# Kernel optimization log

Hardware: AMD Instinct MI355X
Metric: run time of the kernel (lower is better)

## Reference

```python
import jax, jax.numpy as jnp
import numpy as np

N_ENT = 50000
N_REL = 200
DIM = 128
N_BASES = 4
NUM_RELATIONS = 2 * N_REL  # RGCNConv num_relations
E = 200000
S = 20000


def rgcn_conv(x, edge_index, edge_type, edge_norm, basis, att, root, bias, n_nodes):
    """RGCNConv with basis decomposition, aggr='mean'.
    x: [N, Din]; basis: [B, Din, Dout]; att: [R, B]; root: [Din, Dout]; bias: [Dout].
    """
    src, dst = edge_index[0], edge_index[1]
    x_j = x[src]                      # [E, Din] gather
    att_e = att[edge_type]            # [E, B]
    # message: x_j @ (att_e @ basis) without materializing per-edge [Din,Dout] weights
    msg = jnp.einsum('ei,bio,eb->eo', x_j, basis, att_e)  # [E, Dout]
    msg = msg * edge_norm[:, None]
    agg = jax.ops.segment_sum(msg, dst, num_segments=n_nodes)            # [N, Dout]
    cnt = jax.ops.segment_sum(jnp.ones_like(edge_norm), dst, num_segments=n_nodes)
    agg = agg / jnp.maximum(cnt, 1.0)[:, None]            # mean aggregation
    return agg + x @ root + bias


def setup_inputs() -> dict:
    key = jax.random.key(0)
    ks = jax.random.split(key, 20)
    d = {}
    d['entity'] = jnp.arange(N_ENT, dtype=jnp.int64) if jax.config.read('jax_enable_x64') else jnp.arange(N_ENT, dtype=jnp.int32)
    d['edge_index'] = jax.random.randint(ks[0], (2, E), 0, N_ENT)
    d['edge_type'] = jax.random.randint(ks[1], (E,), 0, NUM_RELATIONS)
    d['edge_norm'] = jax.random.uniform(ks[2], (E,), dtype=jnp.float32)
    d['samples'] = jax.random.randint(ks[3], (S, 3), 0, N_REL)
    d['DAD_rel'] = jax.random.normal(ks[4], (N_REL, N_REL), dtype=jnp.float32) * 0.05
    # learned parameters
    d['entity_emb'] = jax.random.normal(ks[5], (N_ENT, DIM), dtype=jnp.float32) * 0.02
    d['relation_emb'] = jax.random.normal(ks[6], (N_REL, DIM), dtype=jnp.float32) * 0.02
    d['entity_context_tab'] = jax.random.normal(ks[7], (N_ENT, DIM), dtype=jnp.float32) * 0.02
    d['relation_context_tab'] = jax.random.normal(ks[8], (N_REL, DIM), dtype=jnp.float32) * 0.02
    d['relation_gcn_weight'] = jax.random.normal(ks[9], (DIM, DIM), dtype=jnp.float32) * 0.02
    d['gate_entity'] = jax.random.uniform(ks[10], (DIM,), dtype=jnp.float32)
    d['gate_relation'] = jax.random.uniform(ks[11], (DIM,), dtype=jnp.float32)
    d['basis1'] = jax.random.normal(ks[12], (N_BASES, DIM, DIM), dtype=jnp.float32) * 0.02
    d['att1'] = jax.random.normal(ks[13], (NUM_RELATIONS, N_BASES), dtype=jnp.float32) * 0.1
    d['root1'] = jax.random.normal(ks[14], (DIM, DIM), dtype=jnp.float32) * 0.02
    d['bias1'] = jnp.zeros((DIM,), dtype=jnp.float32)
    d['basis2'] = jax.random.normal(ks[15], (N_BASES, DIM, DIM), dtype=jnp.float32) * 0.02
    d['att2'] = jax.random.normal(ks[16], (NUM_RELATIONS, N_BASES), dtype=jnp.float32) * 0.1
    d['root2'] = jax.random.normal(ks[17], (DIM, DIM), dtype=jnp.float32) * 0.02
    d['bias2'] = jnp.zeros((DIM,), dtype=jnp.float32)
    return d


def reference(entity, edge_index, edge_type, edge_norm, samples, DAD_rel,
              entity_emb, relation_emb, entity_context_tab, relation_context_tab,
              relation_gcn_weight, gate_entity, gate_relation,
              basis1, att1, root1, bias1, basis2, att2, root2, bias2):
    n_nodes = entity.shape[0]
    ent_ctx = entity_context_tab[entity]                  # [N, D]
    rel_ctx = relation_context_tab                        # arange over all relations -> full table
    ent_ctx = jax.nn.relu(rgcn_conv(ent_ctx, edge_index, edge_type, edge_norm,
                                    basis1, att1, root1, bias1, n_nodes))
    ent_ctx = jax.nn.relu(rgcn_conv(ent_ctx, edge_index, edge_type, edge_norm,
                                    basis2, att2, root2, bias2, n_nodes))
    rel_ctx = jax.nn.relu((DAD_rel @ rel_ctx) @ relation_gcn_weight)
    ge = jax.nn.sigmoid(gate_entity)
    gr = jax.nn.sigmoid(gate_relation)
    h, r, t = samples[:, 0], samples[:, 1], samples[:, 2]
    head_o = ge * entity_emb[h] + (1.0 - ge) * ent_ctx[h]
    rel_o = gr * relation_emb[r] + (1.0 - gr) * rel_ctx[r]
    tail_o = ge * entity_emb[t] + (1.0 - ge) * ent_ctx[t]
    return jnp.stack([head_o, rel_o, tail_o])             # [3, S, D]
```

## Files before the change

### kernel.cpp

```cpp
#include <hip/hip_runtime.h>
#include <hip/hip_bf16.h>

typedef short s8v  __attribute__((ext_vector_type(8)));
typedef float f16v __attribute__((ext_vector_type(16)));

__device__ __forceinline__ unsigned short f2bf(float x) {
    unsigned u = __float_as_uint(x);
    unsigned r = ((u >> 16) & 1u) + 0x7FFFu;
    return (unsigned short)((u + r) >> 16);
}
__device__ __forceinline__ float bf2f(unsigned short h) {
    return __uint_as_float(((unsigned)h) << 16);
}

__global__ __launch_bounds__(256) void prep_kernel(
    const float* __restrict__ basis1, const float* __restrict__ root1,
    const float* __restrict__ basis2, const float* __restrict__ root2,
    unsigned short* __restrict__ Bp1h, unsigned short* __restrict__ Bp2h,
    const int* __restrict__ edge_index, int* __restrict__ deg, int E,
    const float* __restrict__ tab, const int* __restrict__ entity,
    unsigned short* __restrict__ X0h, unsigned short* __restrict__ X0l, int N,
    const float* __restrict__ DAD, const float* __restrict__ rtab,
    const float* __restrict__ Wrel, float* __restrict__ Rc, int NR,
    int b1, int b2, int b3)
{
    __shared__ float smem[384];
    const int b = blockIdx.x, tid = threadIdx.x;

    if (b < b1) {
        float* part = smem;
        float* r1s  = smem + 256;
        int r = b;
        int o = tid & 127, q = tid >> 7;
        float s = 0.f;
        for (int j = q; j < NR; j += 2)
            s = fmaf(DAD[r * NR + j], rtab[j * 128 + o], s);
        part[q * 128 + o] = s;
        __syncthreads();
        if (tid < 128) r1s[tid] = part[tid] + part[128 + tid];
        __syncthreads();
        float s2 = 0.f;
        #pragma unroll 8
        for (int k = q * 64; k < q * 64 + 64; ++k)
            s2 = fmaf(r1s[k], Wrel[k * 128 + o], s2);
        part[q * 128 + o] = s2;
        __syncthreads();
        if (tid < 128)
            Rc[r * 128 + tid] = fmaxf(part[tid] + part[128 + tid], 0.f);
    } else if (b < b2) {
        int bb = b - b1;
        int layer = bb >= 320;
        int idx = (layer ? bb - 320 : bb) * 256 + tid;
        int n = idx & 127, k = idx >> 7;
        const float* basis = layer ? basis2 : basis1;
        const float* root  = layer ? root2  : root1;
        float v = (k < 512) ? basis[((k & 3) << 14) + ((k >> 2) << 7) + n]
                            : root[((k - 512) << 7) + n];
        size_t pos = (((size_t)(k >> 3) * 128) + n) * 8 + (k & 7);
        (layer ? Bp2h : Bp1h)[pos] = f2bf(v);
    } else if (b < b3) {
        int e = (b - b2) * 256 + tid;
        if (e < E) atomicAdd(&deg[edge_index[E + e]], 1);
    } else {
        int idx = (b - b3) * 256 + tid;
        int n = idx >> 5, l = idx & 31;
        if (n < N) {
            int src = entity[n];
            float4 v = *(const float4*)&tab[(size_t)src * 128 + l * 4];
            ushort4 h, lo;
            h.x = f2bf(v.x); lo.x = f2bf(v.x - bf2f(h.x));
            h.y = f2bf(v.y); lo.y = f2bf(v.y - bf2f(h.y));
            h.z = f2bf(v.z); lo.z = f2bf(v.z - bf2f(h.z));
            h.w = f2bf(v.w); lo.w = f2bf(v.w - bf2f(h.w));
            *(ushort4*)&X0h[(size_t)n * 128 + l * 4] = h;
            *(ushort4*)&X0l[(size_t)n * 128 + l * 4] = lo;
        }
    }
}

__global__ __launch_bounds__(1024) void scanA_kernel(
    const int* __restrict__ deg, int* __restrict__ row_start,
    int* __restrict__ btot, int N)
{
    __shared__ int wtot[16];
    __shared__ int woff[16];
    const int tid = threadIdx.x, lane = tid & 63, wid = tid >> 6;
    int i = blockIdx.x * 1024 + tid;
    int v = (i < N) ? deg[i] : 0;
    int x = v;
    #pragma unroll
    for (int d = 1; d < 64; d <<= 1) {
        int t = __shfl_up(x, d, 64);
        if (lane >= d) x += t;
    }
    if (lane == 63) wtot[wid] = x;
    __syncthreads();
    if (wid == 0 && lane < 16) {
        int s = wtot[lane];
        int y = s;
        #pragma unroll
        for (int d = 1; d < 16; d <<= 1) {
            int t = __shfl_up(y, d, 16);
            if (lane >= d) y += t;
        }
        woff[lane] = y - s;
        if (lane == 15) btot[blockIdx.x] = y;
    }
    __syncthreads();
    if (i < N) row_start[i] = woff[wid] + (x - v);
}

__global__ __launch_bounds__(64) void scanB_kernel(
    const int* __restrict__ btot, int* __restrict__ boff,
    int* __restrict__ row_start, int nB, int N)
{
    int t = threadIdx.x;
    int v = (t < nB) ? btot[t] : 0;
    int x = v;
    #pragma unroll
    for (int d = 1; d < 64; d <<= 1) {
        int u = __shfl_up(x, d, 64);
        if (t >= d) x += u;
    }
    if (t < nB) boff[t] = x - v;
    if (t == nB - 1) row_start[N] = x;
}

__global__ __launch_bounds__(1024) void scanC_kernel(
    int* __restrict__ row_start, int* __restrict__ cursor,
    const int* __restrict__ boff, int N)
{
    int i = blockIdx.x * 1024 + threadIdx.x;
    if (i < N) {
        int r = row_start[i] + boff[blockIdx.x];
        row_start[i] = r;
        cursor[i]    = r;
    }
}

__global__ __launch_bounds__(256) void fill_kernel(
    const int* __restrict__ edge_index, const int* __restrict__ edge_type,
    const float* __restrict__ edge_norm, int* __restrict__ cursor,
    const float* __restrict__ att1, const float* __restrict__ att2,
    int* __restrict__ src_s, float4* __restrict__ an1, float4* __restrict__ an2, int E)
{
    int e = blockIdx.x * 256 + threadIdx.x;
    if (e >= E) return;
    int dst = edge_index[E + e];
    int et  = edge_type[e];
    float n = edge_norm[e];
    int pos = atomicAdd(&cursor[dst], 1);
    src_s[pos] = edge_index[e];
    float4 a1 = *(const float4*)&att1[(size_t)et * 4];
    float4 a2 = *(const float4*)&att2[(size_t)et * 4];
    an1[pos] = make_float4(n * a1.x, n * a1.y, n * a1.z, n * a1.w);
    an2[pos] = make_float4(n * a2.x, n * a2.y, n * a2.z, n * a2.w);
}

__global__ __launch_bounds__(256) void layer_kernel(
    const unsigned short* __restrict__ Xh,
    const unsigned short* __restrict__ Xl,
    const int* __restrict__ row_start,
    const int* __restrict__ src_s,
    const float4* __restrict__ an,
    const unsigned short* __restrict__ Bph,
    const float* __restrict__ bias,
    unsigned short* __restrict__ Xoh,
    unsigned short* __restrict__ Xol,
    int N)
{
    __shared__ unsigned short Whi[80 * 32 * 8];
    __shared__ unsigned short Wlo[16 * 32 * 8];

    const int tid   = threadIdx.x;
    const int node0 = blockIdx.x * 32;

    {
        int g = tid >> 5, l = tid & 31;
        int nb = node0 + g * 4;
        int s0a[4], s1a[4];
        #pragma unroll
        for (int i = 0; i < 4; ++i) {
            int gn = nb + i;
            bool ok = gn < N;
            s0a[i] = ok ? row_start[gn] : 0;
            s1a[i] = ok ? row_start[gn + 1] : 0;
        }
        float acc[4][4][4];
        #pragma unroll
        for (int i = 0; i < 4; ++i)
            #pragma unroll
            for (int d = 0; d < 4; ++d)
                #pragma unroll
                for (int c = 0; c < 4; ++c) acc[i][d][c] = 0.f;

        int need = 0;
        #pragma unroll
        for (int i = 0; i < 4; ++i) need = max(need, s1a[i] - s0a[i]);

        for (int p = 0; p < need; p += 4) {
            #pragma unroll
            for (int i = 0; i < 4; ++i) {
                int q0 = s0a[i] + p;
                if (q0 < s1a[i]) {
                    int se = s1a[i] - 1;
                    int q1 = min(q0 + 1, se);
                    int q2 = min(q0 + 2, se);
                    int q3 = min(q0 + 3, se);
                    int sA = src_s[q0], sB = src_s[q1];
                    int sC = src_s[q2], sD = src_s[q3];
                    float4 aA = an[q0], aB = an[q1];
                    float4 aC = an[q2], aD = an[q3];
                    if (q0 + 1 > se) aB = make_float4(0.f, 0.f, 0.f, 0.f);
                    if (q0 + 2 > se) aC = make_float4(0.f, 0.f, 0.f, 0.f);
                    if (q0 + 3 > se) aD = make_float4(0.f, 0.f, 0.f, 0.f);
                    ushort4 hA = *(const ushort4*)&Xh[(size_t)sA * 128 + (l << 2)];
                    ushort4 hB = *(const ushort4*)&Xh[(size_t)sB * 128 + (l << 2)];
                    ushort4 hC = *(const ushort4*)&Xh[(size_t)sC * 128 + (l << 2)];
                    ushort4 hD = *(const ushort4*)&Xh[(size_t)sD * 128 + (l << 2)];
                    float xsA[4] = {bf2f(hA.x), bf2f(hA.y), bf2f(hA.z), bf2f(hA.w)};
                    float xsB[4] = {bf2f(hB.x), bf2f(hB.y), bf2f(hB.z), bf2f(hB.w)};
                    float xsC[4] = {bf2f(hC.x), bf2f(hC.y), bf2f(hC.z), bf2f(hC.w)};
                    float xsD[4] = {bf2f(hD.x), bf2f(hD.y), bf2f(hD.z), bf2f(hD.w)};
                    #pragma unroll
                    for (int d = 0; d < 4; ++d) {
                        acc[i][d][0] = fmaf(aA.x, xsA[d], fmaf(aB.x, xsB[d], fmaf(aC.x, xsC[d], fmaf(aD.x, xsD[d], acc[i][d][0]))));
                        acc[i][d][1] = fmaf(aA.y, xsA[d], fmaf(aB.y, xsB[d], fmaf(aC.y, xsC[d], fmaf(aD.y, xsD[d], acc[i][d][1]))));
                        acc[i][d][2] = fmaf(aA.z, xsA[d], fmaf(aB.z, xsB[d], fmaf(aC.z, xsC[d], fmaf(aD.z, xsD[d], acc[i][d][2]))));
                        acc[i][d][3] = fmaf(aA.w, xsA[d], fmaf(aB.w, xsB[d], fmaf(aC.w, xsC[d], fmaf(aD.w, xsD[d], acc[i][d][3]))));
                    }
                }
            }
        }
        #pragma unroll
        for (int i = 0; i < 4; ++i) {
            int n = g * 4 + i;
            float inv = 1.0f / fmaxf((float)(s1a[i] - s0a[i]), 1.0f);
            #pragma unroll
            for (int d = 0; d < 4; ++d) {
                int kh   = 2 * l + (d >> 1);
                int slot = n ^ (kh & 31);
                ushort4 h;
                h.x = f2bf(acc[i][d][0] * inv);
                h.y = f2bf(acc[i][d][1] * inv);
                h.z = f2bf(acc[i][d][2] * inv);
                h.w = f2bf(acc[i][d][3] * inv);
                *(ushort4*)&Whi[(kh * 32 + slot) * 8 + (d & 1) * 4] = h;
            }
        }
    }

    {
        int r  = tid >> 3;
        int kq = (tid & 7) * 16;
        int gn = node0 + r;
        #pragma unroll
        for (int i = 0; i < 2; ++i) {
            int kh   = 64 + (tid & 7) * 2 + i;
            int slot = r ^ (kh & 31);
            s8v h8 = {0,0,0,0,0,0,0,0}, l8 = {0,0,0,0,0,0,0,0};
            if (gn < N) {
                h8 = *(const s8v*)&Xh[(size_t)gn * 128 + kq + i * 8];
                l8 = *(const s8v*)&Xl[(size_t)gn * 128 + kq + i * 8];
            }
            *(s8v*)&Whi[(kh * 32 + slot) * 8] = h8;
            *(s8v*)&Wlo[((kh - 64) * 32 + slot) * 8] = l8;
        }
    }
    __syncthreads();

    const int lane = tid & 63, wv = tid >> 6;
    const int m    = lane & 31;
    const int kh8  = lane >> 5;
    const int c0   = wv << 5;

    f16v acc;
    #pragma unroll
    for (int i = 0; i < 16; ++i) acc[i] = 0.f;

    s8v Bb[2][4];
    auto loadB4 = [&](int g, int buf) {
        #pragma unroll
        for (int q = 0; q < 4; ++q) {
            int khg = (g * 4 + q) * 2 + kh8;
            size_t off = ((size_t)khg * 128 + c0 + m) * 8;
            Bb[buf][q] = *(const s8v*)&Bph[off];
        }
    };
    loadB4(0, 0);

    #pragma unroll
    for (int g = 0; g < 10; ++g) {
        int buf = g & 1;
        if (g < 9) loadB4(g + 1, buf ^ 1);
        #pragma unroll
        for (int q = 0; q < 4; ++q) {
            int s    = g * 4 + q;
            int khg  = s * 2 + kh8;
            int slot = m ^ (khg & 31);
            s8v aH = *(const s8v*)&Whi[(khg * 32 + slot) * 8];
            if (s >= 32) {
                s8v aL = *(const s8v*)&Wlo[((khg - 64) * 32 + slot) * 8];
                acc = __builtin_amdgcn_mfma_f32_32x32x16_bf16(aL, Bb[buf][q], acc, 0, 0, 0);
            }
            acc = __builtin_amdgcn_mfma_f32_32x32x16_bf16(aH, Bb[buf][q], acc, 0, 0, 0);
        }
    }

    int gc = c0 + m;
    float bv = bias[gc];
    const int rbase = kh8 << 2;
    #pragma unroll
    for (int reg = 0; reg < 16; ++reg) {
        int gr = node0 + rbase + (reg & 3) + ((reg >> 2) << 3);
        if (gr < N) {
            float v = fmaxf(acc[reg] + bv, 0.f);
            unsigned short h = f2bf(v);
            Xoh[(size_t)gr * 128 + gc] = h;
            Xol[(size_t)gr * 128 + gc] = f2bf(v - bf2f(h));
        }
    }
}

__global__ __launch_bounds__(256) void output_kernel(
    const int* __restrict__ samples,
    const float* __restrict__ gate_e,
    const float* __restrict__ gate_r,
    const float* __restrict__ ent_emb,
    const float* __restrict__ rel_emb,
    const unsigned short* __restrict__ ctx2h,
    const unsigned short* __restrict__ ctx2l,
    const float* __restrict__ relctx,
    float* __restrict__ out, int S)
{
    int s = blockIdx.x * 2 + (threadIdx.x >> 7);
    if (s >= S) return;
    int p = blockIdx.y;
    int o = threadIdx.x & 127;
    float v;
    if (p == 1) {
        int idx = samples[s * 3 + 1];
        float g = 1.0f / (1.0f + __expf(-gate_r[o]));
        v = g * rel_emb[idx * 128 + o] + (1.0f - g) * relctx[idx * 128 + o];
    } else {
        int idx = samples[s * 3 + (p == 0 ? 0 : 2)];
        float g = 1.0f / (1.0f + __expf(-gate_e[o]));
        float c = bf2f(ctx2h[(size_t)idx * 128 + o]) + bf2f(ctx2l[(size_t)idx * 128 + o]);
        v = g * ent_emb[(size_t)idx * 128 + o] + (1.0f - g) * c;
    }
    out[(size_t)p * S * 128 + (size_t)s * 128 + o] = v;
}

extern "C" void kernel_launch(void* const* d_in, const int* in_sizes, int n_in,
                              void* d_out, int out_size, void* d_ws, size_t ws_size,
                              hipStream_t stream)
{
    const int*   entity     = (const int*)d_in[0];
    const int*   edge_index = (const int*)d_in[1];
    const int*   edge_type  = (const int*)d_in[2];
    const float* edge_norm  = (const float*)d_in[3];
    const int*   samples    = (const int*)d_in[4];
    const float* DAD        = (const float*)d_in[5];
    const float* ent_emb    = (const float*)d_in[6];
    const float* rel_emb    = (const float*)d_in[7];
    const float* ent_tab    = (const float*)d_in[8];
    const float* rel_tab    = (const float*)d_in[9];
    const float* Wrel       = (const float*)d_in[10];
    const float* gate_e     = (const float*)d_in[11];
    const float* gate_r     = (const float*)d_in[12];
    const float* basis1     = (const float*)d_in[13];
    const float* att1       = (const float*)d_in[14];
    const float* root1      = (const float*)d_in[15];
    const float* bias1      = (const float*)d_in[16];
    const float* basis2     = (const float*)d_in[17];
    const float* att2       = (const float*)d_in[18];
    const float* root2      = (const float*)d_in[19];
    const float* bias2      = (const float*)d_in[20];

    const int N  = in_sizes[0];
    const int E  = in_sizes[2];
    const int S  = in_sizes[4] / 3;
    const int NR = in_sizes[9] / 128;

    unsigned short* X0h = (unsigned short*)d_ws;
    unsigned short* X0l = X0h + (size_t)N * 128;
    unsigned short* X1h = X0l + (size_t)N * 128;
    unsigned short* X1l = X1h + (size_t)N * 128;
    float4* an1    = (float4*)(X1l + (size_t)N * 128);
    float4* an2    = an1 + (E + 4);
    float* Rc      = (float*)(an2 + (E + 4));
    int*   deg     = (int*)(Rc + (size_t)NR * 128);
    int*   rstart  = deg + N;
    int*   cursor  = rstart + N + 1;
    int*   src_s   = cursor + N;
    int*   btot    = src_s + E + 4;
    int*   boff    = btot + 64;
    uintptr_t bt   = ((uintptr_t)(boff + 64) + 15) & ~(uintptr_t)15;
    unsigned short* Bp1h = (unsigned short*)bt;
    unsigned short* Bp2h = Bp1h + 80 * 128 * 8;

    const int egrid = (E + 255) / 256;
    const int lgrid = (N + 31) / 32;
    const int nB    = (N + 1023) / 1024;
    const int x0blocks = (N * 32 + 255) / 256;
    const int b1 = NR;
    const int b2 = NR + 640;
    const int b3 = b2 + egrid;
    const int pgrid = b3 + x0blocks;

    hipMemsetAsync(deg, 0, (size_t)N * sizeof(int), stream);
    prep_kernel<<<pgrid, 256, 0, stream>>>(
        basis1, root1, basis2, root2, Bp1h, Bp2h,
        edge_index, deg, E, ent_tab, entity, X0h, X0l, N,
        DAD, rel_tab, Wrel, Rc, NR, b1, b2, b3);
    scanA_kernel<<<nB, 1024, 0, stream>>>(deg, rstart, btot, N);
    scanB_kernel<<<1, 64, 0, stream>>>(btot, boff, rstart, nB, N);
    scanC_kernel<<<nB, 1024, 0, stream>>>(rstart, cursor, boff, N);
    fill_kernel<<<egrid, 256, 0, stream>>>(edge_index, edge_type, edge_norm, cursor,
                                           att1, att2, src_s, an1, an2, E);

    layer_kernel<<<lgrid, 256, 0, stream>>>(X0h, X0l, rstart, src_s, an1,
                                            Bp1h, bias1, X1h, X1l, N);
    layer_kernel<<<lgrid, 256, 0, stream>>>(X1h, X1l, rstart, src_s, an2,
                                            Bp2h, bias2, X0h, X0l, N);

    output_kernel<<<dim3((S + 1) / 2, 3), 256, 0, stream>>>(
        samples, gate_e, gate_r, ent_emb, rel_emb, X0h, X0l, Rc, (float*)d_out, S);
}
```

Before: 292.6 us.

## Fuse scan phases, move X0 conversion into fill kernel, keep root operand in registers

Merges the single-block scanB into scanC, so every block recomputes the block-offset prefix from btot itself and one launch is removed. The X0 gather and bf16 hi/lo split moves from prep into fill_kernel, using 16-byte writes per thread. In layer_kernel, each lane loads the self-node hi/lo operand for the root matmul straight from global into registers instead of staging it in LDS. This shrinks shared memory and drops a staging pass, at the cost of more registers per thread and different load coalescing.

Result: slower. 307.5 us (+5.1%).

```diff
diff --git a/kernel.cpp b/kernel.cpp
--- a/kernel.cpp
+++ b/kernel.cpp
@@ -18,11 +18,9 @@
     const float* __restrict__ basis2, const float* __restrict__ root2,
     unsigned short* __restrict__ Bp1h, unsigned short* __restrict__ Bp2h,
     const int* __restrict__ edge_index, int* __restrict__ deg, int E,
-    const float* __restrict__ tab, const int* __restrict__ entity,
-    unsigned short* __restrict__ X0h, unsigned short* __restrict__ X0l, int N,
     const float* __restrict__ DAD, const float* __restrict__ rtab,
     const float* __restrict__ Wrel, float* __restrict__ Rc, int NR,
-    int b1, int b2, int b3)
+    int b1, int b2)
 {
     __shared__ float smem[384];
     const int b = blockIdx.x, tid = threadIdx.x;
@@ -58,23 +56,9 @@
                             : root[((k - 512) << 7) + n];
         size_t pos = (((size_t)(k >> 3) * 128) + n) * 8 + (k & 7);
         (layer ? Bp2h : Bp1h)[pos] = f2bf(v);
-    } else if (b < b3) {
+    } else {
         int e = (b - b2) * 256 + tid;
         if (e < E) atomicAdd(&deg[edge_index[E + e]], 1);
-    } else {
-        int idx = (b - b3) * 256 + tid;
-        int n = idx >> 5, l = idx & 31;
-        if (n < N) {
-            int src = entity[n];
-            float4 v = *(const float4*)&tab[(size_t)src * 128 + l * 4];
-            ushort4 h, lo;
-            h.x = f2bf(v.x); lo.x = f2bf(v.x - bf2f(h.x));
-            h.y = f2bf(v.y); lo.y = f2bf(v.y - bf2f(h.y));
-            h.z = f2bf(v.z); lo.z = f2bf(v.z - bf2f(h.z));
-            h.w = f2bf(v.w); lo.w = f2bf(v.w - bf2f(h.w));
-            *(ushort4*)&X0h[(size_t)n * 128 + l * 4] = h;
-            *(ushort4*)&X0l[(size_t)n * 128 + l * 4] = lo;
-        }
     }
 }
 
@@ -110,51 +94,75 @@
     if (i < N) row_start[i] = woff[wid] + (x - v);
 }
 
-__global__ __launch_bounds__(64) void scanB_kernel(
-    const int* __restrict__ btot, int* __restrict__ boff,
-    int* __restrict__ row_start, int nB, int N)
-{
-    int t = threadIdx.x;
-    int v = (t < nB) ? btot[t] : 0;
-    int x = v;
-    #pragma unroll
-    for (int d = 1; d < 64; d <<= 1) {
-        int u = __shfl_up(x, d, 64);
-        if (t >= d) x += u;
-    }
-    if (t < nB) boff[t] = x - v;
-    if (t == nB - 1) row_start[N] = x;
-}
-
 __global__ __launch_bounds__(1024) void scanC_kernel(
     int* __restrict__ row_start, int* __restrict__ cursor,
-    const int* __restrict__ boff, int N)
-{
-    int i = blockIdx.x * 1024 + threadIdx.x;
+    const int* __restrict__ btot, int nB, int N)
+{
+    __shared__ int incl[64];
+    const int tid = threadIdx.x;
+    if (tid < 64) {
+        int v = (tid < nB) ? btot[tid] : 0;
+        int x = v;
+        #pragma unroll
+        for (int d = 1; d < 64; d <<= 1) {
+            int t = __shfl_up(x, d, 64);
+            if (tid >= d) x += t;
+        }
+        incl[tid] = x;
+    }
+    __syncthreads();
+    int off = (blockIdx.x == 0) ? 0 : incl[blockIdx.x - 1];
+    int i = blockIdx.x * 1024 + tid;
     if (i < N) {
-        int r = row_start[i] + boff[blockIdx.x];
+        int r = row_start[i] + off;
         row_start[i] = r;
         cursor[i]    = r;
     }
+    if (blockIdx.x == (unsigned)(nB - 1) && tid == 0)
+        row_start[N] = incl[nB - 1];
 }
 
 __global__ __launch_bounds__(256) void fill_kernel(
     const int* __restrict__ edge_index, const int* __restrict__ edge_type,
     const float* __restrict__ edge_norm, int* __restrict__ cursor,
     const float* __restrict__ att1, const float* __restrict__ att2,
-    int* __restrict__ src_s, float4* __restrict__ an1, float4* __restrict__ an2, int E)
-{
-    int e = blockIdx.x * 256 + threadIdx.x;
-    if (e >= E) return;
-    int dst = edge_index[E + e];
-    int et  = edge_type[e];
-    float n = edge_norm[e];
-    int pos = atomicAdd(&cursor[dst], 1);
-    src_s[pos] = edge_index[e];
-    float4 a1 = *(const float4*)&att1[(size_t)et * 4];
-    float4 a2 = *(const float4*)&att2[(size_t)et * 4];
-    an1[pos] = make_float4(n * a1.x, n * a1.y, n * a1.z, n * a1.w);
-    an2[pos] = make_float4(n * a2.x, n * a2.y, n * a2.z, n * a2.w);
+    int* __restrict__ src_s, float4* __restrict__ an1, float4* __restrict__ an2, int E,
+    const float* __restrict__ tab, const int* __restrict__ entity,
+    unsigned short* __restrict__ X0h, unsigned short* __restrict__ X0l, int N,
+    int fblocks)
+{
+    const int b = blockIdx.x, tid = threadIdx.x;
+    if (b < fblocks) {
+        int e = b * 256 + tid;
+        if (e >= E) return;
+        int dst = edge_index[E + e];
+        int et  = edge_type[e];
+        float n = edge_norm[e];
+        int pos = atomicAdd(&cursor[dst], 1);
+        src_s[pos] = edge_index[e];
+        float4 a1 = *(const float4*)&att1[(size_t)et * 4];
+        float4 a2 = *(const float4*)&att2[(size_t)et * 4];
+        an1[pos] = make_float4(n * a1.x, n * a1.y, n * a1.z, n * a1.w);
+        an2[pos] = make_float4(n * a2.x, n * a2.y, n * a2.z, n * a2.w);
+    } else {
+        int idx = (b - fblocks) * 256 + tid;
+        int nn = idx >> 4, part = idx & 15;
+        if (nn < N) {
+            int src = entity[nn];
+            const float4* sp = (const float4*)&tab[(size_t)src * 128 + part * 8];
+            float4 v0 = sp[0], v1 = sp[1];
+            float vs[8] = {v0.x, v0.y, v0.z, v0.w, v1.x, v1.y, v1.z, v1.w};
+            s8v h8, l8;
+            #pragma unroll
+            for (int j = 0; j < 8; ++j) {
+                unsigned short h = f2bf(vs[j]);
+                h8[j] = (short)h;
+                l8[j] = (short)f2bf(vs[j] - bf2f(h));
+            }
+            *(s8v*)&X0h[(size_t)nn * 128 + part * 8] = h8;
+            *(s8v*)&X0l[(size_t)nn * 128 + part * 8] = l8;
+        }
+    }
 }
 
 __global__ __launch_bounds__(256) void layer_kernel(
@@ -169,8 +177,7 @@
     unsigned short* __restrict__ Xol,
     int N)
 {
-    __shared__ unsigned short Whi[80 * 32 * 8];
-    __shared__ unsigned short Wlo[16 * 32 * 8];
+    __shared__ unsigned short Whi[64 * 32 * 8];
 
     const int tid   = threadIdx.x;
     const int node0 = blockIdx.x * 32;
@@ -250,39 +257,42 @@
         }
     }
 
-    {
-        int r  = tid >> 3;
-        int kq = (tid & 7) * 16;
-        int gn = node0 + r;
-        #pragma unroll
-        for (int i = 0; i < 2; ++i) {
-            int kh   = 64 + (tid & 7) * 2 + i;
-            int slot = r ^ (kh & 31);
-            s8v h8 = {0,0,0,0,0,0,0,0}, l8 = {0,0,0,0,0,0,0,0};
-            if (gn < N) {
-                h8 = *(const s8v*)&Xh[(size_t)gn * 128 + kq + i * 8];
-                l8 = *(const s8v*)&Xl[(size_t)gn * 128 + kq + i * 8];
-            }
-            *(s8v*)&Whi[(kh * 32 + slot) * 8] = h8;
-            *(s8v*)&Wlo[((kh - 64) * 32 + slot) * 8] = l8;
-        }
-    }
-    __syncthreads();
-
     const int lane = tid & 63, wv = tid >> 6;
     const int m    = lane & 31;
     const int kh8  = lane >> 5;
-    const int c0   = wv << 5;
+    const s8v z8 = {0, 0, 0, 0, 0, 0, 0, 0};
+    s8v xh[8], xl[8];
+    {
+        int gn  = node0 + m;
+        bool ok = gn < N;
+        size_t xbase = (size_t)(ok ? gn : 0) * 128;
+        #pragma unroll
+        for (int q = 0; q < 8; ++q) {
+            int dk = 2 * q + kh8;
+            xh[q] = *(const s8v*)&Xh[xbase + dk * 8];
+            xl[q] = *(const s8v*)&Xl[xbase + dk * 8];
+        }
+        if (!ok) {
+            #pragma unroll
+            for (int q = 0; q < 8; ++q) { xh[q] = z8; xl[q] = z8; }
+        }
+    }
+    __syncthreads();
+
+    const int c0 = wv << 5;
 
     f16v acc;
     #pragma unroll
     for (int i = 0; i < 16; ++i) acc[i] = 0.f;
 
     s8v Bb[2][4];
+    auto khg_of = [&](int t) {
+        return (t < 8) ? (64 + 2 * t + kh8) : (2 * (t - 8) + kh8);
+    };
     auto loadB4 = [&](int g, int buf) {
         #pragma unroll
         for (int q = 0; q < 4; ++q) {
-            int khg = (g * 4 + q) * 2 + kh8;
+            int khg = khg_of(g * 4 + q);
             size_t off = ((size_t)khg * 128 + c0 + m) * 8;
             Bb[buf][q] = *(const s8v*)&Bph[off];
         }
@@ -295,15 +305,16 @@
         if (g < 9) loadB4(g + 1, buf ^ 1);
         #pragma unroll
         for (int q = 0; q < 4; ++q) {
-            int s    = g * 4 + q;
-            int khg  = s * 2 + kh8;
-            int slot = m ^ (khg & 31);
-            s8v aH = *(const s8v*)&Whi[(khg * 32 + slot) * 8];
-            if (s >= 32) {
-                s8v aL = *(const s8v*)&Wlo[((khg - 64) * 32 + slot) * 8];
-                acc = __builtin_amdgcn_mfma_f32_32x32x16_bf16(aL, Bb[buf][q], acc, 0, 0, 0);
+            int t = g * 4 + q;
+            if (t < 8) {
+                acc = __builtin_amdgcn_mfma_f32_32x32x16_bf16(xl[t], Bb[buf][q], acc, 0, 0, 0);
+                acc = __builtin_amdgcn_mfma_f32_32x32x16_bf16(xh[t], Bb[buf][q], acc, 0, 0, 0);
+            } else {
+                int khg  = 2 * (t - 8) + kh8;
+                int slot = m ^ (khg & 31);
+                s8v aH = *(const s8v*)&Whi[(khg * 32 + slot) * 8];
+                acc = __builtin_amdgcn_mfma_f32_32x32x16_bf16(aH, Bb[buf][q], acc, 0, 0, 0);
             }
-            acc = __builtin_amdgcn_mfma_f32_32x32x16_bf16(aH, Bb[buf][q], acc, 0, 0, 0);
         }
     }
 
@@ -402,22 +413,21 @@
     const int egrid = (E + 255) / 256;
     const int lgrid = (N + 31) / 32;
     const int nB    = (N + 1023) / 1024;
-    const int x0blocks = (N * 32 + 255) / 256;
+    const int x0blocks = (N * 16 + 255) / 256;
     const int b1 = NR;
     const int b2 = NR + 640;
-    const int b3 = b2 + egrid;
-    const int pgrid = b3 + x0blocks;
+    const int pgrid = b2 + egrid;
 
     hipMemsetAsync(deg, 0, (size_t)N * sizeof(int), stream);
     prep_kernel<<<pgrid, 256, 0, stream>>>(
         basis1, root1, basis2, root2, Bp1h, Bp2h,
-        edge_index, deg, E, ent_tab, entity, X0h, X0l, N,
-        DAD, rel_tab, Wrel, Rc, NR, b1, b2, b3);
+        edge_index, deg, E,
+        DAD, rel_tab, Wrel, Rc, NR, b1, b2);
     scanA_kernel<<<nB, 1024, 0, stream>>>(deg, rstart, btot, N);
-    scanB_kernel<<<1, 64, 0, stream>>>(btot, boff, rstart, nB, N);
-    scanC_kernel<<<nB, 1024, 0, stream>>>(rstart, cursor, boff, N);
-    fill_kernel<<<egrid, 256, 0, stream>>>(edge_index, edge_type, edge_norm, cursor,
-                                           att1, att2, src_s, an1, an2, E);
+    scanC_kernel<<<nB, 1024, 0, stream>>>(rstart, cursor, btot, nB, N);
+    fill_kernel<<<egrid + x0blocks, 256, 0, stream>>>(
+        edge_index, edge_type, edge_norm, cursor, att1, att2, src_s, an1, an2, E,
+        ent_tab, entity, X0h, X0l, N, egrid);
 
     layer_kernel<<<lgrid, 256, 0, stream>>>(X0h, X0l, rstart, src_s, an1,
                                             Bp1h, bias1, X1h, X1l, N);
```
